# Performance work log

Hardware: AMD Instinct MI355X
Metric: run time of the kernel (lower is better)

Reference implementation:

```python
import jax, jax.numpy as jnp
import numpy as np

B, SEQ, NF = 16, 512, 32
E, HID, PRED = 128, 512, 96
N_FFT, HOP, TOPM = 64, 32, 32
W = SEQ // HOP + 1          # 17 windows (centered STFT)
F = N_FFT // 2 + 1          # 33 onesided freqs
LAM = 0.01                  # sparsity_threshold (softshrink)
SCALE = 0.02


def _hann(n):
    # periodic hann, matches torch.hann_window default
    return 0.5 - 0.5 * jnp.cos(2.0 * jnp.pi * jnp.arange(n) / n)


def _softshrink(v):
    return jnp.sign(v) * jnp.maximum(jnp.abs(v) - LAM, 0.0)


def setup_inputs():
    key = jax.random.key(0)
    ks = jax.random.split(key, 12)
    d = {}
    d['x'] = jax.random.normal(ks[0], (B, SEQ, NF), jnp.float32)
    d['embeddings'] = jax.random.normal(ks[1], (1, E), jnp.float32)
    for nm, k in zip(['Wr', 'Wi', 'Wrl', 'Wil', 'Wrr', 'Wir'], ks[2:8]):
        d[nm] = SCALE * jax.random.normal(k, (W, E, E), jnp.float32)
    d['br'] = SCALE * jax.random.normal(ks[8], (W, E), jnp.float32)
    d['bi'] = SCALE * jax.random.normal(ks[9], (W, E), jnp.float32)
    d['fc_w1'] = SCALE * jax.random.normal(ks[10], (SEQ * E, HID), jnp.float32)
    d['fc_b1'] = jnp.zeros((HID,), jnp.float32)
    d['fc_w2'] = SCALE * jax.random.normal(ks[11], (HID, PRED), jnp.float32)
    d['fc_b2'] = jnp.zeros((PRED,), jnp.float32)
    return d


def _forward(x, embeddings, Wr, Wi, Wrl, Wil, Wrr, Wir, br, bi,
             fc_w1, fc_b1, fc_w2, fc_b2):
    Bq, T, N = x.shape
    # tokenEmb: (B,T,N) -> (B,N,T,E)
    xe = x.transpose(0, 2, 1)[..., None] * embeddings
    bias = xe
    # ---- STFT (centered, reflect pad, hann, onesided) ----
    xt = xe.transpose(0, 1, 3, 2)                      # (B,N,E,T)
    pad = N_FFT // 2
    xp = jnp.pad(xt, ((0, 0), (0, 0), (0, 0), (pad, pad)), mode='reflect')
    win = _hann(N_FFT).astype(x.dtype)
    idx = jnp.arange(W)[:, None] * HOP + jnp.arange(N_FFT)[None, :]  # (W,nfft)
    frames = xp[..., idx] * win                        # (B,N,E,W,nfft)
    spec = jnp.fft.rfft(frames, axis=-1)               # (B,N,E,W,F)
    spec = spec.transpose(0, 1, 3, 4, 2)               # (B,N,W,F,E)
    # ---- top-M frequency select (dim=3) ----
    sm = jnp.moveaxis(spec, 3, -1)                     # (B,N,W,E,F)
    _, top_idx = jax.lax.top_k(jnp.abs(sm), TOPM)      # (B,N,W,E,M)
    vals = jnp.take_along_axis(sm, top_idx, axis=-1)
    xw = jnp.moveaxis(vals, -1, 3)                     # (B,N,W,M,E)
    # ---- per-window complex MLP with left/right neighbor windows ----
    z0 = jnp.zeros_like(xw[:, :, :1])
    xl = jnp.concatenate([z0, xw[:, :, :-1]], axis=2)  # left neighbor (zero at w=0)
    xr = jnp.concatenate([xw[:, :, 1:], z0], axis=2)   # right neighbor (zero at w=W-1)

    def cmul(z, wr, wi):
        re = jnp.einsum('bnwme,wef->bnwmf', z.real, wr) - jnp.einsum('bnwme,wef->bnwmf', z.imag, wi)
        im = jnp.einsum('bnwme,wef->bnwmf', z.imag, wr) + jnp.einsum('bnwme,wef->bnwmf', z.real, wi)
        return re, im

    re_m, im_m = cmul(xw, Wr, Wi)
    re_l, im_l = cmul(xl, Wrl, Wil)
    re_r, im_r = cmul(xr, Wrr, Wir)
    o_re = jax.nn.relu(re_m + re_l + re_r + br[None, None, :, None, :])
    o_im = jax.nn.relu(im_m + im_l + im_r + bi[None, None, :, None, :])
    y = _softshrink(o_re) + 1j * _softshrink(o_im)     # (B,N,W,M,E) complex
    # ---- scatter-pad back to full frequency grid ----
    ym = jnp.moveaxis(y, 3, -1)                        # (B,N,W,E,M)
    K = Bq * N * W * E
    flat_vals = ym.reshape(K, TOPM)
    flat_idx = top_idx.reshape(K, TOPM)
    full = jnp.zeros((K, F), ym.dtype).at[jnp.arange(K)[:, None], flat_idx].set(flat_vals)
    spec_full = jnp.moveaxis(full.reshape(Bq, N, W, E, F), -1, 3)  # (B,N,W,F,E)
    # ---- ISTFT (windowed OLA / window-squared envelope, centered trim) ----
    sf = spec_full.transpose(0, 1, 4, 2, 3)            # (B,N,E,W,F)
    fr = jnp.fft.irfft(sf, n=N_FFT, axis=-1) * win     # (B,N,E,W,nfft)
    L = (W - 1) * HOP + N_FFT
    ola = jnp.zeros((Bq, N, E, L), fr.dtype).at[..., idx].add(fr)
    env = jnp.zeros((L,), win.dtype).at[idx].add(win * win)
    ola = ola / jnp.where(env > 1e-11, env, 1.0)
    xt2 = ola[..., pad:L - pad]                        # (B,N,E,T)
    xo = xt2.transpose(0, 1, 3, 2) + bias              # (B,N,T,E) + residual
    # ---- fc head ----
    h = xo.reshape(Bq, N, T * E)
    h = jax.nn.leaky_relu(h @ fc_w1 + fc_b1, 0.01)
    out = h @ fc_w2 + fc_b2                            # (B,N,PRED)
    return out.transpose(0, 2, 1)                      # (B,PRED,N)


def reference(x, embeddings, Wr, Wi, Wrl, Wil, Wrr, Wir, br, bi,
              fc_w1, fc_b1, fc_w2, fc_b2):
    return _forward(x, embeddings, Wr, Wi, Wrl, Wil, Wrr, Wir, br, bi,
                    fc_w1, fc_b1, fc_w2, fc_b2)
```

## Files before the change

kernel.cpp:

```cpp
#include <hip/hip_runtime.h>
#include <hip/hip_bf16.h>

#define LAM 0.01f

typedef __attribute__((ext_vector_type(8))) short v8s;
typedef __attribute__((ext_vector_type(4))) float v4f;

static __device__ __forceinline__ unsigned short f2bf(float f) {
    union { float f; unsigned int u; } v; v.f = f;
    unsigned int u = v.u;
    u += 0x7fffu + ((u >> 16) & 1u);
    return (unsigned short)(u >> 16);
}
static __device__ __forceinline__ float bf2f(unsigned short h) {
    union { unsigned int u; float f; } c; c.u = ((unsigned int)h) << 16;
    return c.f;
}

static __device__ __forceinline__ void async16(const void* g, void* l) {
    __builtin_amdgcn_global_load_lds(
        (const __attribute__((address_space(1))) unsigned int*)g,
        (__attribute__((address_space(3))) unsigned int*)l, 16, 0, 0);
}

#define OFF_COEF 0ull
#define OFF_V    69632ull
#define OFF_BINS 2297856ull
#define OFF_AIMG 3411968ull
#define OFF_W1P  70520832ull
#define OFF_HP   137629696ull

__global__ __launch_bounds__(128) void coef_kernel(
    const float* __restrict__ emb,
    const float* __restrict__ Wr, const float* __restrict__ Wi,
    const float* __restrict__ Wrl, const float* __restrict__ Wil,
    const float* __restrict__ Wrr, const float* __restrict__ Wir,
    const float* __restrict__ br, const float* __restrict__ bi,
    float* __restrict__ coef)
{
    int w = blockIdx.x, j = blockIdx.y, e = threadIdx.x;
    float out;
    if (j < 6) {
        const float* Wj;
        switch (j) {
            case 0: Wj = Wr; break; case 1: Wj = Wi; break;
            case 2: Wj = Wrl; break; case 3: Wj = Wil; break;
            case 4: Wj = Wrr; break; default: Wj = Wir; break;
        }
        const float* p = Wj + (size_t)w * 16384 + e;
        float acc = 0.f;
        #pragma unroll 8
        for (int ep = 0; ep < 128; ++ep) acc = fmaf(emb[ep], p[ep * 128], acc);
        out = acc;
    } else if (j == 6) {
        out = br[w * 128 + e] - LAM;
    } else {
        out = bi[w * 128 + e] - LAM;
    }
    coef[((size_t)(w * 128 + e)) * 8 + j] = out;
}

__global__ __launch_bounds__(256) void stft_kernel(
    const float* __restrict__ x, float2* __restrict__ V, int* __restrict__ bins)
{
    __shared__ float sig[576];
    __shared__ float winT[64];
    __shared__ float2 tw[64];
    __shared__ float2 Sbuf[17 * 33];
    __shared__ float absb[17 * 33];

    const int blk = blockIdx.x;
    const int b = blk >> 5, n = blk & 31;
    const int tid = threadIdx.x;
    const float C64 = 0.09817477042468103f;

    if (tid < 64) {
        float ang = (float)tid * C64;
        winT[tid] = 0.5f - 0.5f * cosf(ang);
        tw[tid] = make_float2(cosf(ang), sinf(ang));
    }
    for (int l = tid; l < 576; l += 256) {
        int t = (l < 32) ? (32 - l) : ((l < 544) ? (l - 32) : (1054 - l));
        sig[l] = x[(size_t)b * 16384 + t * 32 + n];
    }
    __syncthreads();

    for (int task = tid; task < 561; task += 256) {
        int w = task / 33, f = task - w * 33;
        float sr = 0.f, si = 0.f;
        int base = w * 32;
        for (int t = 0; t < 64; ++t) {
            float sw = sig[base + t] * winT[t];
            float2 cs = tw[(f * t) & 63];
            sr = fmaf(sw, cs.x, sr);
            si = fmaf(sw, -cs.y, si);
        }
        Sbuf[task] = make_float2(sr, si);
        absb[task] = sqrtf(fmaf(sr, sr, si * si));
    }
    __syncthreads();

    for (int task = tid; task < 561; task += 256) {
        int w = task / 33, f = task - w * 33;
        float a = absb[task];
        int base = w * 33, rank = 0;
        for (int j = 0; j < 33; ++j) {
            float aj = absb[base + j];
            rank += (aj > a) || (aj == a && j < f);
        }
        if (rank < 32) {
            size_t o = ((size_t)blk * 17 + w) * 32 + rank;
            V[o] = Sbuf[task];
            bins[o] = f;
        }
    }
}

__global__ __launch_bounds__(256) void cvt_kernel(
    const float* __restrict__ w1, unsigned short* __restrict__ w1p)
{
    __shared__ float T[32][132];
    const int kb = blockIdx.x, nt = blockIdx.y;
    const int tid = threadIdx.x;

    #pragma unroll
    for (int p = 0; p < 4; ++p) {
        int r = (tid >> 5) + p * 8;
        int c = (tid & 31) * 4;
        float4 v = *(const float4*)&w1[((size_t)(kb * 32 + r)) * 512 + nt * 128 + c];
        T[r][c] = v.x; T[r][c + 1] = v.y; T[r][c + 2] = v.z; T[r][c + 3] = v.w;
    }
    __syncthreads();

    unsigned short* dst = w1p + ((size_t)nt * 2048 + kb) * 4096;
    #pragma unroll
    for (int p = 0; p < 2; ++p) {
        int pos = tid + 256 * p;
        int np = pos >> 2, cs = pos & 3;
        int clog = cs ^ ((np >> 2) & 3);
        unsigned int pk[4];
        #pragma unroll
        for (int j2 = 0; j2 < 4; ++j2) {
            unsigned short lo = f2bf(T[clog * 8 + j2 * 2][np]);
            unsigned short hi = f2bf(T[clog * 8 + j2 * 2 + 1][np]);
            pk[j2] = (unsigned int)lo | ((unsigned int)hi << 16);
        }
        *(uint4*)&dst[pos * 8] = make_uint4(pk[0], pk[1], pk[2], pk[3]);
    }
}

#define MID_ROLL(J0, J1, J2, J3)                                                \
    {                                                                           \
        _Pragma("unroll") for (int e2 = 0; e2 < 2; ++e2)                        \
        _Pragma("unroll") for (int i = 0; i < 4; ++i) {                         \
            roll[e2][J0][i] = fmaf(acc[0][e2][i], win16[0][i], roll[e2][J0][i]);\
            roll[e2][J1][i] = fmaf(acc[1][e2][i], win16[1][i], roll[e2][J1][i]);\
            roll[e2][J2][i] = fmaf(acc[2][e2][i], win16[2][i], roll[e2][J2][i]);\
            roll[e2][J3][i] = fmaf(acc[3][e2][i], win16[3][i], roll[e2][J3][i]);\
        }                                                                       \
    }

#define MID_FLUSH(JJA, JJB)                                                     \
    {                                                                           \
        _Pragma("unroll") for (int i = 0; i < 4; ++i) {                         \
            int tp = 32 * (w - 1) + q * 4 + i;                                  \
            float xb = xs[tp];                                                  \
            _Pragma("unroll") for (int e2 = 0; e2 < 2; ++e2) {                  \
                float val = fmaf(roll[e2][JJA][i], renv[0][i], xb * emb2[e2]);  \
                Aimg[cbase[e2] + (size_t)tp * 16384] = f2bf(val);               \
                roll[e2][JJA][i] = 0.f;                                         \
            }                                                                   \
            int tp2 = tp + 16;                                                  \
            float xb2 = xs[tp2];                                                \
            _Pragma("unroll") for (int e2 = 0; e2 < 2; ++e2) {                  \
                float val = fmaf(roll[e2][JJB][i], renv[1][i], xb2 * emb2[e2]); \
                Aimg[cbase[e2] + (size_t)tp2 * 16384] = f2bf(val);              \
                roll[e2][JJB][i] = 0.f;                                         \
            }                                                                   \
        }                                                                       \
    }

__global__ __launch_bounds__(256) void mid_kernel(
    const float* __restrict__ x, const float* __restrict__ emb,
    const float* __restrict__ coef, const float2* __restrict__ V,
    const int* __restrict__ bins, unsigned short* __restrict__ Aimg)
{
    __shared__ unsigned short M1t[64 * 72];
    __shared__ unsigned short Yt[128 * 72];
    __shared__ float cosT[64];
    __shared__ float sinT[64];
    __shared__ float2 Vs[17 * 32];
    __shared__ int Bns[17 * 32];
    __shared__ float xs[512];

    const int blk = blockIdx.x;
    const int b = blk >> 5, n = blk & 31;
    const int tid = threadIdx.x;
    const int wave = tid >> 6, lane = tid & 63, l15 = lane & 15, q = lane >> 4;
    const float C64 = 0.09817477042468103f;

    if (tid < 64) {
        float ang = (float)tid * C64;
        cosT[tid] = __cosf(ang);
        sinT[tid] = __sinf(ang);
    }
    {
        const float2* Vg = V + (size_t)blk * 544;
        const int* Bg = bins + (size_t)blk * 544;
        for (int i = tid; i < 544; i += 256) { Vs[i] = Vg[i]; Bns[i] = Bg[i]; }
        for (int i = tid; i < 512; i += 256) xs[i] = x[(size_t)b * 16384 + i * 32 + n];
    }

    float win16[4][4];
    #pragma unroll
    for (int tt = 0; tt < 4; ++tt)
        #pragma unroll
        for (int i = 0; i < 4; ++i) {
            int t = tt * 16 + q * 4 + i;
            win16[tt][i] = 0.5f - 0.5f * __cosf((float)t * C64);
        }
    float renv[2][4];
    #pragma unroll
    for (int hf = 0; hf < 2; ++hf)
        #pragma unroll
        for (int i = 0; i < 4; ++i) {
            int k = hf * 16 + q * 4 + i;
            float w0 = 0.5f - 0.5f * __cosf((float)k * C64);
            float w1v = 0.5f - 0.5f * __cosf((float)(k + 32) * C64);
            renv[hf][i] = 1.0f / (w0 * w0 + w1v * w1v);
        }
    int ebase[2];
    float emb2[2];
    size_t cbase[2];
    const int mt = blk >> 7, mp = blk & 127, s = (mp >> 2) & 3;
    #pragma unroll
    for (int e2 = 0; e2 < 2; ++e2) {
        ebase[e2] = (wave * 2 + e2) * 16 + l15;
        emb2[e2] = emb[ebase[e2]];
        int e = ebase[e2];
        int echunk = e >> 5, clog = (e >> 3) & 3, cs = clog ^ s, el = e & 7;
        cbase[e2] = ((size_t)mt * 2048 + echunk) * 4096 + mp * 32 + cs * 8 + el;
    }

    float roll[2][4][4];
    #pragma unroll
    for (int e2 = 0; e2 < 2; ++e2)
        #pragma unroll
        for (int jj = 0; jj < 4; ++jj)
            #pragma unroll
            for (int i = 0; i < 4; ++i) roll[e2][jj][i] = 0.f;

    const int e1 = tid & 127;
    const int mg = (tid >> 7) << 4;
    const int tM = tid & 63;
    const int kg = wave << 4;

    __syncthreads();

    for (int w = 0; w < 17; ++w) {
        {
            const float4* cf = (const float4*)(coef + ((size_t)(w * 128 + e1)) * 8);
            float4 cA = cf[0];
            float4 cB = cf[1];
            unsigned int rep[8], imp[8];
            #pragma unroll
            for (int j2 = 0; j2 < 8; ++j2) {
                unsigned int rpack = 0, ipack = 0;
                #pragma unroll
                for (int sdx = 0; sdx < 2; ++sdx) {
                    int m = mg + j2 * 2 + sdx;
                    float2 vm = Vs[w * 32 + m];
                    float2 vl = (w > 0) ? Vs[(w - 1) * 32 + m] : make_float2(0.f, 0.f);
                    float2 vp = (w < 16) ? Vs[(w + 1) * 32 + m] : make_float2(0.f, 0.f);
                    float re = cB.z;
                    re = fmaf(vm.x, cA.x, re); re = fmaf(-vm.y, cA.y, re);
                    re = fmaf(vl.x, cA.z, re); re = fmaf(-vl.y, cA.w, re);
                    re = fmaf(vp.x, cB.x, re); re = fmaf(-vp.y, cB.y, re);
                    float im = cB.w;
                    im = fmaf(vm.y, cA.x, im); im = fmaf(vm.x, cA.y, im);
                    im = fmaf(vl.y, cA.z, im); im = fmaf(vl.x, cA.w, im);
                    im = fmaf(vp.y, cB.x, im); im = fmaf(vp.x, cB.y, im);
                    re = fmaxf(re, 0.f);
                    im = fmaxf(im, 0.f);
                    rpack |= (unsigned int)f2bf(re) << (16 * sdx);
                    ipack |= (unsigned int)f2bf(im) << (16 * sdx);
                }
                rep[j2] = rpack; imp[j2] = ipack;
            }
            uint4* dr = (uint4*)&Yt[e1 * 72 + mg];
            dr[0] = make_uint4(rep[0], rep[1], rep[2], rep[3]);
            dr[1] = make_uint4(rep[4], rep[5], rep[6], rep[7]);
            uint4* di = (uint4*)&Yt[e1 * 72 + 32 + mg];
            di[0] = make_uint4(imp[0], imp[1], imp[2], imp[3]);
            di[1] = make_uint4(imp[4], imp[5], imp[6], imp[7]);
        }
        {
            unsigned int mpk[8];
            #pragma unroll
            for (int j2 = 0; j2 < 8; ++j2) {
                unsigned int pk = 0;
                #pragma unroll
                for (int sdx = 0; sdx < 2; ++sdx) {
                    int k = kg + j2 * 2 + sdx;
                    int m = k & 31;
                    int r = Bns[w * 32 + m];
                    float sc = (r == 0 || r == 32) ? 0.015625f : 0.03125f;
                    int idx = (r * tM) & 63;
                    float val = (k < 32) ? (cosT[idx] * sc) : (-sinT[idx] * sc);
                    pk |= (unsigned int)f2bf(val) << (16 * sdx);
                }
                mpk[j2] = pk;
            }
            uint4* dm = (uint4*)&M1t[tM * 72 + kg];
            dm[0] = make_uint4(mpk[0], mpk[1], mpk[2], mpk[3]);
            dm[1] = make_uint4(mpk[4], mpk[5], mpk[6], mpk[7]);
        }
        __syncthreads();

        v4f acc[4][2];
        #pragma unroll
        for (int tt = 0; tt < 4; ++tt)
            #pragma unroll
            for (int e2 = 0; e2 < 2; ++e2) acc[tt][e2] = (v4f){0.f, 0.f, 0.f, 0.f};
        #pragma unroll
        for (int ks = 0; ks < 2; ++ks) {
            v8s bfr[2];
            #pragma unroll
            for (int e2 = 0; e2 < 2; ++e2)
                bfr[e2] = *(const v8s*)&Yt[ebase[e2] * 72 + ks * 32 + q * 8];
            #pragma unroll
            for (int tt = 0; tt < 4; ++tt) {
                v8s af = *(const v8s*)&M1t[(tt * 16 + l15) * 72 + ks * 32 + q * 8];
                #pragma unroll
                for (int e2 = 0; e2 < 2; ++e2)
                    acc[tt][e2] = __builtin_amdgcn_mfma_f32_16x16x32_bf16(
                        af, bfr[e2], acc[tt][e2], 0, 0, 0);
            }
        }

        if ((w & 1) == 0) {
            MID_ROLL(0, 1, 2, 3);
            if (w > 0) {
                MID_FLUSH(0, 1);
            } else {
                #pragma unroll
                for (int e2 = 0; e2 < 2; ++e2)
                    #pragma unroll
                    for (int i = 0; i < 4; ++i) {
                        roll[e2][0][i] = 0.f; roll[e2][1][i] = 0.f;
                    }
            }
        } else {
            MID_ROLL(2, 3, 0, 1);
            MID_FLUSH(2, 3);
        }
        __syncthreads();
    }
}

__global__ __launch_bounds__(512) void gemm_kernel(
    const unsigned short* __restrict__ Aimg, const unsigned short* __restrict__ w1p,
    unsigned short* __restrict__ hp, int iters)
{
    __shared__ unsigned short As[2][8192];
    __shared__ unsigned short Bs[2][8192];

    const int tid = threadIdx.x;
    const int mt2 = blockIdx.x >> 1, nt2 = blockIdx.x & 1;
    const int ks = blockIdx.y;
    const int wave = tid >> 6, lane = tid & 63;
    const int l15 = lane & 15, q = lane >> 4;
    const int kb0 = ks * iters;

    const int isB = wave >> 2;
    const int sub = wave & 3;
    const unsigned short* gsrc = (isB
        ? w1p + ((size_t)(nt2 * 2 + (sub >> 1)) * 2048 + kb0) * 4096
        : Aimg + ((size_t)(mt2 * 2 + (sub >> 1)) * 2048 + kb0) * 4096)
        + (sub & 1) * 2048 + lane * 8;
    const int ldsoff = (sub >> 1) * 4096 + (sub & 1) * 2048;

    v4f acc[4][8];
    #pragma unroll
    for (int mf = 0; mf < 4; ++mf)
        #pragma unroll
        for (int nf = 0; nf < 8; ++nf) acc[mf][nf] = (v4f){0.f, 0.f, 0.f, 0.f};

    {
        unsigned short* dst = (isB ? Bs[0] : As[0]) + ldsoff;
        #pragma unroll
        for (int j = 0; j < 4; ++j) async16(gsrc + j * 512, dst + j * 512);
    }

    const int wm = wave >> 1, wn = wave & 1;
    const int ca = (q ^ ((l15 >> 2) & 3)) * 8;
    const int rA = (wm >> 1) * 4096 + ((wm & 1) * 64 + l15) * 32 + ca;
    const int rB = wn * 4096 + l15 * 32 + ca;

    for (int it = 0; it < iters; ++it) {
        __syncthreads();
        if (it + 1 < iters) {
            const unsigned short* src = gsrc + (size_t)(it + 1) * 4096;
            unsigned short* dst = (isB ? Bs[(it + 1) & 1] : As[(it + 1) & 1]) + ldsoff;
            #pragma unroll
            for (int j = 0; j < 4; ++j) async16(src + j * 512, dst + j * 512);
        }
        const int cur = it & 1;
        v8s af[4], bf[8];
        #pragma unroll
        for (int f = 0; f < 4; ++f) af[f] = *(const v8s*)&As[cur][rA + f * 512];
        #pragma unroll
        for (int nf = 0; nf < 8; ++nf) bf[nf] = *(const v8s*)&Bs[cur][rB + nf * 512];
        #pragma unroll
        for (int mf = 0; mf < 4; ++mf)
            #pragma unroll
            for (int nf = 0; nf < 8; ++nf)
                acc[mf][nf] = __builtin_amdgcn_mfma_f32_16x16x32_bf16(
                    af[mf], bf[nf], acc[mf][nf], 0, 0, 0);
    }

    #pragma unroll
    for (int mf = 0; mf < 4; ++mf)
        #pragma unroll
        for (int nf = 0; nf < 8; ++nf) {
            int row = mt2 * 256 + wm * 64 + mf * 16 + q * 4;
            int col = nt2 * 256 + wn * 128 + nf * 16 + l15;
            unsigned short* dst = hp + ((size_t)ks * 512 + row) * 512 + col;
            #pragma unroll
            for (int i = 0; i < 4; ++i) dst[(size_t)i * 512] = f2bf(acc[mf][nf][i]);
        }
}

__global__ __launch_bounds__(128) void reduce_kernel(
    const unsigned short* __restrict__ hp, const float* __restrict__ b1,
    float* __restrict__ h, int KS)
{
    const int g = blockIdx.x * 128 + threadIdx.x;
    const uint4* base = (const uint4*)hp + g;

    float acc[8];
    #pragma unroll
    for (int j = 0; j < 8; ++j) acc[j] = 0.f;

    #pragma unroll 8
    for (int k = 0; k < KS; ++k) {
        uint4 v = base[(size_t)k * 32768];
        acc[0] += bf2f((unsigned short)(v.x & 0xffff));
        acc[1] += bf2f((unsigned short)(v.x >> 16));
        acc[2] += bf2f((unsigned short)(v.y & 0xffff));
        acc[3] += bf2f((unsigned short)(v.y >> 16));
        acc[4] += bf2f((unsigned short)(v.z & 0xffff));
        acc[5] += bf2f((unsigned short)(v.z >> 16));
        acc[6] += bf2f((unsigned short)(v.w & 0xffff));
        acc[7] += bf2f((unsigned short)(v.w >> 16));
    }

    const int flat = g * 8;
    const int hid = flat & 511;
    float4 o0, o1;
    float* po = (float*)&o0;
    #pragma unroll
    for (int j = 0; j < 8; ++j) {
        float s = acc[j] + b1[hid + j];
        ((float*)&o0)[0];
        float r = (s > 0.f) ? s : 0.01f * s;
        if (j < 4) ((float*)&o0)[j] = r; else ((float*)&o1)[j - 4] = r;
    }
    *(float4*)&h[flat] = o0;
    *(float4*)&h[flat + 4] = o1;
}

__global__ __launch_bounds__(128) void fcmat_kernel(
    const float* __restrict__ h, const float* __restrict__ w2,
    const float* __restrict__ b2, float* __restrict__ out)
{
    __shared__ float hbuf[512];
    const int row = blockIdx.x;
    const int tid = threadIdx.x;
    #pragma unroll
    for (int ii = 0; ii < 4; ++ii)
        hbuf[tid + ii * 128] = h[(size_t)row * 512 + tid + ii * 128];
    __syncthreads();
    if (tid < 96) {
        float a = b2[tid];
        #pragma unroll 8
        for (int hh = 0; hh < 512; ++hh) a = fmaf(hbuf[hh], w2[hh * 96 + tid], a);
        int b = row >> 5, n = row & 31;
        out[(size_t)b * 3072 + tid * 32 + n] = a;
    }
}

extern "C" void kernel_launch(void* const* d_in, const int* in_sizes, int n_in,
                              void* d_out, int out_size, void* d_ws, size_t ws_size,
                              hipStream_t stream) {
    const float* x   = (const float*)d_in[0];
    const float* emb = (const float*)d_in[1];
    const float* Wr  = (const float*)d_in[2];
    const float* Wi  = (const float*)d_in[3];
    const float* Wrl = (const float*)d_in[4];
    const float* Wil = (const float*)d_in[5];
    const float* Wrr = (const float*)d_in[6];
    const float* Wir = (const float*)d_in[7];
    const float* br  = (const float*)d_in[8];
    const float* bi  = (const float*)d_in[9];
    const float* w1  = (const float*)d_in[10];
    const float* b1  = (const float*)d_in[11];
    const float* w2  = (const float*)d_in[12];
    const float* b2  = (const float*)d_in[13];

    char* ws = (char*)d_ws;
    float* coef          = (float*)(ws + OFF_COEF);
    float2* V            = (float2*)(ws + OFF_V);
    int* bins            = (int*)(ws + OFF_BINS);
    unsigned short* Aimg = (unsigned short*)(ws + OFF_AIMG);
    unsigned short* w1p  = (unsigned short*)(ws + OFF_W1P);
    unsigned short* hpp  = (unsigned short*)(ws + OFF_HP);

    int KS = 64;
    size_t hp_bytes = (size_t)KS * 512 * 512 * 2;
    if (OFF_HP + hp_bytes + (1ull << 20) > ws_size) {
        KS = 32; hp_bytes = (size_t)KS * 512 * 512 * 2;
    }
    int iters = 2048 / KS;
    float* hbase = (float*)(ws + OFF_HP + hp_bytes);

    coef_kernel<<<dim3(17, 8), dim3(128), 0, stream>>>(
        emb, Wr, Wi, Wrl, Wil, Wrr, Wir, br, bi, coef);
    cvt_kernel<<<dim3(2048, 4), dim3(256), 0, stream>>>(w1, w1p);
    stft_kernel<<<dim3(512), dim3(256), 0, stream>>>(x, V, bins);
    mid_kernel<<<dim3(512), dim3(256), 0, stream>>>(x, emb, coef, V, bins, Aimg);
    gemm_kernel<<<dim3(4, KS), dim3(512), 0, stream>>>(Aimg, w1p, hpp, iters);
    reduce_kernel<<<dim3(256), dim3(128), 0, stream>>>(hpp, b1, hbase, KS);
    fcmat_kernel<<<dim3(512), dim3(128), 0, stream>>>(hbase, w2, b2, (float*)d_out);
}
```

Baseline: 417.8 us.

## Split mid kernel over window halves, remap GEMM blocks per XCD, fuse reduce into fc2

The mid kernel now launches twice as many blocks, each covering 9 of the 17 windows, with one window of overlap so the rolling overlap-add state can restart. This doubles parallelism but recomputes the boundary window. The GEMM grid is flattened and block IDs are remapped so that split-K slices sharing operands land on the same XCD, aiming at better L2 reuse. The split-K reduction, bias and leaky-relu are fused into the fc2 kernel, which removes one launch and the intermediate h buffer; the workspace headroom check is relaxed to match.

```diff
diff --git a/kernel.cpp b/kernel.cpp
--- a/kernel.cpp
+++ b/kernel.cpp
@@ -193,7 +193,9 @@
     __shared__ int Bns[17 * 32];
     __shared__ float xs[512];
 
-    const int blk = blockIdx.x;
+    const int blk2 = blockIdx.x;
+    const int blk = blk2 & 511;
+    const int wbeg = (blk2 >> 9) * 8;
     const int b = blk >> 5, n = blk & 31;
     const int tid = threadIdx.x;
     const int wave = tid >> 6, lane = tid & 63, l15 = lane & 15, q = lane >> 4;
@@ -257,7 +259,7 @@
 
     __syncthreads();
 
-    for (int w = 0; w < 17; ++w) {
+    for (int w = wbeg; w < wbeg + 9; ++w) {
         {
             const float4* cf = (const float4*)(coef + ((size_t)(w * 128 + e1)) * 8);
             float4 cA = cf[0];
@@ -340,7 +342,7 @@
 
         if ((w & 1) == 0) {
             MID_ROLL(0, 1, 2, 3);
-            if (w > 0) {
+            if (w > wbeg) {
                 MID_FLUSH(0, 1);
             } else {
                 #pragma unroll
@@ -360,14 +362,22 @@
 
 __global__ __launch_bounds__(512) void gemm_kernel(
     const unsigned short* __restrict__ Aimg, const unsigned short* __restrict__ w1p,
-    unsigned short* __restrict__ hp, int iters)
+    unsigned short* __restrict__ hp, int iters, int KS)
 {
     __shared__ unsigned short As[2][8192];
     __shared__ unsigned short Bs[2][8192];
 
+    const int gid = blockIdx.x;
+    const int xcd = gid & 7;
+    const int u = gid >> 3;
+    const int KS4 = KS >> 2;
+    const int nt2 = (u >= KS4) ? 1 : 0;
+    const int vv = u - nt2 * KS4;
+    const int pid = vv * 8 + xcd;
+    const int ks = pid >> 1;
+    const int mt2 = pid & 1;
+
     const int tid = threadIdx.x;
-    const int mt2 = blockIdx.x >> 1, nt2 = blockIdx.x & 1;
-    const int ks = blockIdx.y;
     const int wave = tid >> 6, lane = tid & 63;
     const int l15 = lane & 15, q = lane >> 4;
     const int kb0 = ks * iters;
@@ -431,60 +441,33 @@
         }
 }
 
-__global__ __launch_bounds__(128) void reduce_kernel(
+__global__ __launch_bounds__(256) void fc2_kernel(
     const unsigned short* __restrict__ hp, const float* __restrict__ b1,
-    float* __restrict__ h, int KS)
-{
-    const int g = blockIdx.x * 128 + threadIdx.x;
-    const uint4* base = (const uint4*)hp + g;
-
-    float acc[8];
-    #pragma unroll
-    for (int j = 0; j < 8; ++j) acc[j] = 0.f;
-
-    #pragma unroll 8
-    for (int k = 0; k < KS; ++k) {
-        uint4 v = base[(size_t)k * 32768];
-        acc[0] += bf2f((unsigned short)(v.x & 0xffff));
-        acc[1] += bf2f((unsigned short)(v.x >> 16));
-        acc[2] += bf2f((unsigned short)(v.y & 0xffff));
-        acc[3] += bf2f((unsigned short)(v.y >> 16));
-        acc[4] += bf2f((unsigned short)(v.z & 0xffff));
-        acc[5] += bf2f((unsigned short)(v.z >> 16));
-        acc[6] += bf2f((unsigned short)(v.w & 0xffff));
-        acc[7] += bf2f((unsigned short)(v.w >> 16));
-    }
-
-    const int flat = g * 8;
-    const int hid = flat & 511;
-    float4 o0, o1;
-    float* po = (float*)&o0;
-    #pragma unroll
-    for (int j = 0; j < 8; ++j) {
-        float s = acc[j] + b1[hid + j];
-        ((float*)&o0)[0];
-        float r = (s > 0.f) ? s : 0.01f * s;
-        if (j < 4) ((float*)&o0)[j] = r; else ((float*)&o1)[j - 4] = r;
-    }
-    *(float4*)&h[flat] = o0;
-    *(float4*)&h[flat + 4] = o1;
-}
-
-__global__ __launch_bounds__(128) void fcmat_kernel(
-    const float* __restrict__ h, const float* __restrict__ w2,
-    const float* __restrict__ b2, float* __restrict__ out)
+    const float* __restrict__ w2, const float* __restrict__ b2,
+    float* __restrict__ out, int KS)
 {
     __shared__ float hbuf[512];
     const int row = blockIdx.x;
     const int tid = threadIdx.x;
-    #pragma unroll
-    for (int ii = 0; ii < 4; ++ii)
-        hbuf[tid + ii * 128] = h[(size_t)row * 512 + tid + ii * 128];
+
+    const unsigned int* base = (const unsigned int*)(hp + (size_t)row * 512) + tid;
+    float a0 = 0.f, a1 = 0.f;
+    #pragma unroll 8
+    for (int k = 0; k < KS; ++k) {
+        unsigned int v = base[(size_t)k * 131072];
+        a0 += bf2f((unsigned short)(v & 0xffff));
+        a1 += bf2f((unsigned short)(v >> 16));
+    }
+    float s0 = a0 + b1[tid * 2];
+    float s1 = a1 + b1[tid * 2 + 1];
+    hbuf[tid * 2]     = (s0 > 0.f) ? s0 : 0.01f * s0;
+    hbuf[tid * 2 + 1] = (s1 > 0.f) ? s1 : 0.01f * s1;
     __syncthreads();
+
     if (tid < 96) {
         float a = b2[tid];
         #pragma unroll 8
-        for (int hh = 0; hh < 512; ++hh) a = fmaf(hbuf[hh], w2[hh * 96 + tid], a);
+        for (int h = 0; h < 512; ++h) a = fmaf(hbuf[h], w2[h * 96 + tid], a);
         int b = row >> 5, n = row & 31;
         out[(size_t)b * 3072 + tid * 32 + n] = a;
     }
@@ -518,18 +501,16 @@
 
     int KS = 64;
     size_t hp_bytes = (size_t)KS * 512 * 512 * 2;
-    if (OFF_HP + hp_bytes + (1ull << 20) > ws_size) {
+    if (OFF_HP + hp_bytes > ws_size) {
         KS = 32; hp_bytes = (size_t)KS * 512 * 512 * 2;
     }
     int iters = 2048 / KS;
-    float* hbase = (float*)(ws + OFF_HP + hp_bytes);
 
     coef_kernel<<<dim3(17, 8), dim3(128), 0, stream>>>(
         emb, Wr, Wi, Wrl, Wil, Wrr, Wir, br, bi, coef);
     cvt_kernel<<<dim3(2048, 4), dim3(256), 0, stream>>>(w1, w1p);
     stft_kernel<<<dim3(512), dim3(256), 0, stream>>>(x, V, bins);
-    mid_kernel<<<dim3(512), dim3(256), 0, stream>>>(x, emb, coef, V, bins, Aimg);
-    gemm_kernel<<<dim3(4, KS), dim3(512), 0, stream>>>(Aimg, w1p, hpp, iters);
-    reduce_kernel<<<dim3(256), dim3(128), 0, stream>>>(hpp, b1, hbase, KS);
-    fcmat_kernel<<<dim3(512), dim3(128), 0, stream>>>(hbase, w2, b2, (float*)d_out);
-}
+    mid_kernel<<<dim3(1024), dim3(256), 0, stream>>>(x, emb, coef, V, bins, Aimg);
+    gemm_kernel<<<dim3(4 * KS), dim3(512), 0, stream>>>(Aimg, w1p, hpp, iters, KS);
+    fc2_kernel<<<dim3(512), dim3(256), 0, stream>>>(hpp, b1, w2, b2, (float*)d_out, KS);
+}
```

Result: no change. 417.4 us (-0.1%).
